# Optimization experiments

Measured on AMD Instinct MI355X. Metric: run time of the kernel, lower is better.

Reference implementation:

```python
import jax, jax.numpy as jnp
import numpy as np

NUM_HEADS = 16
KEY_SIZE = 64
HEAD_SIZE = 64


def setup_inputs() -> dict:
    key = jax.random.key(0)
    ks = jax.random.split(key, 8)
    B, S, D = 2, 2048, 1024
    s = 1.0 / np.sqrt(D)
    return {
        "q": jax.random.normal(ks[0], (B, S, D), jnp.float32),
        "k": jax.random.normal(ks[1], (B, S, D), jnp.float32),
        "v": jax.random.normal(ks[2], (B, S, D), jnp.float32),
        "v_mask": jax.random.randint(ks[3], (B, S), 0, 2, jnp.int32),
        "Wq": jax.random.normal(ks[4], (D, NUM_HEADS * KEY_SIZE), jnp.float32) * s,
        "Wk": jax.random.normal(ks[5], (D, NUM_HEADS * KEY_SIZE), jnp.float32) * s,
        "Wv": jax.random.normal(ks[6], (D, NUM_HEADS * HEAD_SIZE), jnp.float32) * s,
    }


def reference(q, k, v, v_mask, Wq, Wk, Wv):
    B, Sq, _ = q.shape
    Sk = k.shape[1]
    # projections + split heads: [B, S, H, d]
    qw = (q @ Wq).reshape(B, Sq, NUM_HEADS, KEY_SIZE)
    kw = (k @ Wk).reshape(B, Sk, NUM_HEADS, KEY_SIZE)
    vw = (v @ Wv).reshape(B, Sk, NUM_HEADS, HEAD_SIZE)
    # scores [B, H, Sq, Sk]
    a = jnp.einsum('bqhd,bkhd->bhqk', qw, kw) / np.sqrt(KEY_SIZE).astype(np.float32)
    # additive mask over key axis: x*m - (1-m)*1e12
    m = v_mask.astype(a.dtype)[:, None, None, :]
    a = a * m - (1.0 - m) * 1e12
    a = jax.nn.softmax(a, axis=-1)
    # output [B, Sq, H*head_size]
    o = jnp.einsum('bhqk,bkhd->bqhd', a, vw)
    return o.reshape(B, Sq, NUM_HEADS * HEAD_SIZE)
```

## Files before the change

### kernel.cpp

```cpp
#include <hip/hip_runtime.h>
#include <hip/hip_bf16.h>


#define SEQ 2048
#define DIM 1024
#define NPROJ 1024

typedef __bf16 bf16x8 __attribute__((ext_vector_type(8)));
typedef float floatx4 __attribute__((ext_vector_type(4)));
typedef float floatx16 __attribute__((ext_vector_type(16)));

__device__ inline unsigned short f2bf_bits(float x) {
  __hip_bfloat16 h = __float2bfloat16(x);
  return __builtin_bit_cast(unsigned short, h);
}

__device__ __forceinline__ void gload_lds16(const void* g, void* l) {
  __builtin_amdgcn_global_load_lds((const __attribute__((address_space(1))) void*)g,
                                   (__attribute__((address_space(3))) void*)l, 16, 0, 0);
}

__global__ __launch_bounds__(256) void cvt_x(
    const float* __restrict__ q, const float* __restrict__ k, const float* __restrict__ v,
    unsigned short* __restrict__ xb)
{
  const float* X = blockIdx.z == 0 ? q : (blockIdx.z == 1 ? k : v);
  unsigned short* O = xb + (size_t)blockIdx.z * 4096 * 1024;
  int i0 = blockIdx.x * 256 + threadIdx.x;
  #pragma unroll
  for (int it = 0; it < 4; ++it) {
    int i = i0 + it * 262144;
    float4 f = *reinterpret_cast<const float4*>(&X[(size_t)i * 4]);
    ushort4 o;
    o.x = f2bf_bits(f.x); o.y = f2bf_bits(f.y);
    o.z = f2bf_bits(f.z); o.w = f2bf_bits(f.w);
    *reinterpret_cast<ushort4*>(&O[(size_t)i * 4]) = o;
  }
}

__global__ __launch_bounds__(256) void transpose_w(
    const float* __restrict__ Wq, const float* __restrict__ Wk, const float* __restrict__ Wv,
    unsigned short* __restrict__ WqT, unsigned short* __restrict__ WkT, unsigned short* __restrict__ WvT)
{
  const float* W = blockIdx.z == 0 ? Wq : (blockIdx.z == 1 ? Wk : Wv);
  unsigned short* WT = blockIdx.z == 0 ? WqT : (blockIdx.z == 1 ? WkT : WvT);
  const float sc = (blockIdx.z == 0) ? 0.1803368801f : 1.0f;
  __shared__ float tile[64][65];
  const int k0 = blockIdx.x * 64;
  const int n0 = blockIdx.y * 64;
  const int t = threadIdx.x;
  #pragma unroll
  for (int it = 0; it < 4; ++it) {
    int idx = t + (it << 8);
    int r = idx >> 4, c4 = (idx & 15) << 2;
    float4 v = *reinterpret_cast<const float4*>(&W[(k0 + r) * DIM + n0 + c4]);
    tile[r][c4 + 0] = v.x; tile[r][c4 + 1] = v.y;
    tile[r][c4 + 2] = v.z; tile[r][c4 + 3] = v.w;
  }
  __syncthreads();
  #pragma unroll
  for (int it = 0; it < 4; ++it) {
    int idx = t + (it << 8);
    int r = idx >> 4, c4 = (idx & 15) << 2;
    ushort4 o;
    o.x = f2bf_bits(tile[c4 + 0][r] * sc);
    o.y = f2bf_bits(tile[c4 + 1][r] * sc);
    o.z = f2bf_bits(tile[c4 + 2][r] * sc);
    o.w = f2bf_bits(tile[c4 + 3][r] * sc);
    *reinterpret_cast<ushort4*>(&WT[(n0 + r) * DIM + k0 + c4]) = o;
  }
}

__global__ __launch_bounds__(256, 4) void proj_gemm(
    const unsigned short* __restrict__ xb,
    const unsigned short* __restrict__ WqT, const unsigned short* __restrict__ WkT,
    const unsigned short* __restrict__ WvT,
    unsigned short* __restrict__ qw, unsigned short* __restrict__ kw, unsigned short* __restrict__ vw)
{
  const unsigned short* X = xb + (size_t)blockIdx.z * 4096 * 1024;
  const unsigned short* WT = blockIdx.z == 0 ? WqT : (blockIdx.z == 1 ? WkT : WvT);
  unsigned short* Y = blockIdx.z == 0 ? qw : (blockIdx.z == 1 ? kw : vw);

  __shared__ unsigned short Al[2][128 * 32];
  __shared__ unsigned short Bl[2][128 * 32];

  const int m0 = blockIdx.x * 128, n0 = blockIdx.y * 128;
  const int t = threadIdx.x;
  const int lane = t & 63;
  const int wid = t >> 6;
  const int wm = (wid >> 1) << 6, wn = (wid & 1) << 6;
  const int qd = lane >> 4, ln = lane & 15;

  auto stage = [&](int ks, int bi) {
    const int kb = ks << 6;
    #pragma unroll
    for (int i = 0; i < 2; ++i) {
      int p = t + (i << 8);
      int r = p >> 2, c = p & 3;
      int f = (r + (r >> 2)) & 3;
      gload_lds16((const char*)X + (size_t)(m0 + r) * 2048 + kb + ((c ^ f) << 4),
                  (char*)&Al[bi][0] + p * 16);
      gload_lds16((const char*)WT + (size_t)(n0 + r) * 2048 + kb + ((c ^ f) << 4),
                  (char*)&Bl[bi][0] + p * 16);
    }
  };

  floatx4 acc[4][4] = {};
  stage(0, 0);

  for (int ks = 0; ks < 32; ++ks) {
    __syncthreads();
    if (ks + 1 < 32) stage(ks + 1, (ks + 1) & 1);
    const int bi = ks & 1;
    bf16x8 af[4], bfr[4];
    #pragma unroll
    for (int mb = 0; mb < 4; ++mb) {
      int m = wm + mb * 16 + ln;
      int fm = (m + (m >> 2)) & 3;
      af[mb] = *reinterpret_cast<const bf16x8*>(&Al[bi][m * 32 + ((qd ^ fm) << 3)]);
    }
    #pragma unroll
    for (int nb = 0; nb < 4; ++nb) {
      int n = wn + nb * 16 + ln;
      int fn = (n + (n >> 2)) & 3;
      bfr[nb] = *reinterpret_cast<const bf16x8*>(&Bl[bi][n * 32 + ((qd ^ fn) << 3)]);
    }
    #pragma unroll
    for (int mb = 0; mb < 4; ++mb)
      #pragma unroll
      for (int nb = 0; nb < 4; ++nb)
        acc[mb][nb] = __builtin_amdgcn_mfma_f32_16x16x32_bf16(af[mb], bfr[nb], acc[mb][nb], 0, 0, 0);
  }
  #pragma unroll
  for (int mb = 0; mb < 4; ++mb)
    #pragma unroll
    for (int nb = 0; nb < 4; ++nb)
      #pragma unroll
      for (int i = 0; i < 4; ++i) {
        int m = m0 + wm + mb * 16 + qd * 4 + i;
        int n = n0 + wn + nb * 16 + ln;
        Y[(size_t)m * NPROJ + n] = f2bf_bits(acc[mb][nb][i]);
      }
}

__global__ __launch_bounds__(256) void transpose_v(
    const unsigned short* __restrict__ vw, const int* __restrict__ vmask,
    unsigned short* __restrict__ vt, unsigned short* __restrict__ mb)
{
  if (blockIdx.y == 0 && blockIdx.x < 16) {
    int i = blockIdx.x * 256 + threadIdx.x;
    mb[i] = vmask[i] ? 0x3F80 : 0;
  }
  __shared__ unsigned short tile[64 * 64];
  const int t = threadIdx.x;
  const int s0 = blockIdx.x * 64;
  const int bh = blockIdx.y;
  const int b = bh >> 4, h = bh & 15;
  #pragma unroll
  for (int it = 0; it < 2; ++it) {
    int p = t + (it << 8);
    int s = p >> 3, c = p & 7;
    int cp = (c + (s >> 3) + (s & 7)) & 7;
    int4 d = *reinterpret_cast<const int4*>(&vw[(size_t)(b * SEQ + s0 + s) * NPROJ + h * 64 + c * 8]);
    if (vmask[b * SEQ + s0 + s] == 0) { d.x = 0; d.y = 0; d.z = 0; d.w = 0; }
    *reinterpret_cast<int4*>(&tile[s * 64 + cp * 8]) = d;
  }
  __syncthreads();
  #pragma unroll
  for (int it = 0; it < 2; ++it) {
    int d = (t >> 3) + (it << 5), sc = t & 7;
    struct { alignas(16) unsigned short u[8]; } o;
    #pragma unroll
    for (int j = 0; j < 8; ++j) {
      int s = sc * 8 + j;
      int cp = ((d >> 3) + (s >> 3) + (s & 7)) & 7;
      o.u[j] = tile[s * 64 + cp * 8 + (d & 7)];
    }
    *reinterpret_cast<int4*>(&vt[(size_t)(bh * 64 + d) * SEQ + s0 + sc * 8]) =
        *reinterpret_cast<const int4*>(o.u);
  }
}

__global__ __launch_bounds__(256, 3) void attn_fwd(
    const unsigned short* __restrict__ qw, const unsigned short* __restrict__ kw,
    const unsigned short* __restrict__ vt, const unsigned short* __restrict__ mb,
    float* __restrict__ out)
{
  extern __shared__ char smem[];
  unsigned short* P  = (unsigned short*)smem;
  unsigned short* Kl = (unsigned short*)(smem + 18432);
  unsigned short* Vl = (unsigned short*)(smem + 34816);
  unsigned short* Ml = (unsigned short*)(smem + 51200);

  const int t = threadIdx.x, lane = t & 63, wid = t >> 6;
  const int l5 = lane & 31, hi = lane >> 5;
  const int bh = blockIdx.x;
  const int q0 = blockIdx.y * 128;
  const int b = bh >> 4, h = bh & 15;
  const int base = b * SEQ;
  const int wq = wid * 32;

  auto stage = [&](int kt, int bi) {
    const int k0 = kt << 6;
    #pragma unroll
    for (int i = 0; i < 2; ++i) {
      int rb = wid * 16 + i * 8;
      int r = rb + (lane >> 3);
      int sw = ((lane & 7) ^ (r & 7)) << 4;
      gload_lds16((const char*)kw + ((size_t)((base + k0 + r) * NPROJ + h * 64) << 1) + sw,
                  (char*)&Kl[bi * 4096] + rb * 128);
      gload_lds16((const char*)vt + ((size_t)((bh * 64 + r) * SEQ + k0) << 1) + sw,
                  (char*)&Vl[bi * 4096] + rb * 128);
    }
    if (wid == 3 && lane < 8)
      gload_lds16((const char*)mb + ((size_t)(base + k0 + lane * 8) << 1), (char*)&Ml[bi * 64]);
  };

  #pragma unroll
  for (int i = 0; i < 4; ++i) {
    int idx = t + (i << 8);
    int r = idx >> 3, c8 = (idx & 7) << 3;
    *reinterpret_cast<int4*>(&P[r * 72 + c8]) =
        *reinterpret_cast<const int4*>(&qw[(size_t)((base + q0 + r) * NPROJ + h * 64 + c8)]);
  }
  __syncthreads();
  bf16x8 qf[4];
  #pragma unroll
  for (int kk = 0; kk < 4; ++kk)
    qf[kk] = *reinterpret_cast<const bf16x8*>(&P[(wq + l5) * 72 + kk * 16 + hi * 8]);

  floatx16 oa0 = {}, oa1 = {}, la = {};
  stage(0, 0);

  #pragma unroll 2
  for (int kt = 0; kt < SEQ / 64; ++kt) {
    __syncthreads();
    if (kt + 1 < SEQ / 64) stage(kt + 1, (kt + 1) & 1);
    const int bi = kt & 1;

    floatx16 s0 = {}, s1 = {};
    #pragma unroll
    for (int kk = 0; kk < 4; ++kk) {
      int ph = ((kk * 2 + hi) ^ (l5 & 7)) << 3;
      bf16x8 b0 = *reinterpret_cast<const bf16x8*>(&Kl[bi * 4096 + l5 * 64 + ph]);
      bf16x8 b1 = *reinterpret_cast<const bf16x8*>(&Kl[bi * 4096 + (32 + l5) * 64 + ph]);
      s0 = __builtin_amdgcn_mfma_f32_32x32x16_bf16(qf[kk], b0, s0, 0, 0, 0);
      s1 = __builtin_amdgcn_mfma_f32_32x32x16_bf16(qf[kk], b1, s1, 0, 0, 0);
    }

    #pragma unroll
    for (int r = 0; r < 16; ++r) {
      float p0 = __builtin_amdgcn_exp2f(s0[r]);
      float p1 = __builtin_amdgcn_exp2f(s1[r]);
      int row = wq + (r & 3) + ((r >> 2) << 3) + (hi << 2);
      P[row * 72 + l5] = f2bf_bits(p0);
      P[row * 72 + 32 + l5] = f2bf_bits(p1);
    }

    #pragma unroll
    for (int kk = 0; kk < 4; ++kk) {
      bf16x8 ap = *reinterpret_cast<const bf16x8*>(&P[(wq + l5) * 72 + kk * 16 + hi * 8]);
      int ph = ((kk * 2 + hi) ^ (l5 & 7)) << 3;
      bf16x8 v0 = *reinterpret_cast<const bf16x8*>(&Vl[bi * 4096 + l5 * 64 + ph]);
      bf16x8 v1 = *reinterpret_cast<const bf16x8*>(&Vl[bi * 4096 + (32 + l5) * 64 + ph]);
      bf16x8 mf = *reinterpret_cast<const bf16x8*>(&Ml[bi * 64 + kk * 16 + hi * 8]);
      oa0 = __builtin_amdgcn_mfma_f32_32x32x16_bf16(ap, v0, oa0, 0, 0, 0);
      oa1 = __builtin_amdgcn_mfma_f32_32x32x16_bf16(ap, v1, oa1, 0, 0, 0);
      la  = __builtin_amdgcn_mfma_f32_32x32x16_bf16(ap, mf, la, 0, 0, 0);
    }
  }

  #pragma unroll
  for (int r = 0; r < 16; ++r) {
    int row = wq + (r & 3) + ((r >> 2) << 3) + (hi << 2);
    float inv = 1.0f / la[r];
    size_t o = (size_t)(base + q0 + row) * NPROJ + h * 64;
    out[o + l5] = oa0[r] * inv;
    out[o + 32 + l5] = oa1[r] * inv;
  }
}

extern "C" void kernel_launch(void* const* d_in, const int* in_sizes, int n_in,
                              void* d_out, int out_size, void* d_ws, size_t ws_size,
                              hipStream_t stream) {
  const float* q  = (const float*)d_in[0];
  const float* k  = (const float*)d_in[1];
  const float* v  = (const float*)d_in[2];
  const int* vm   = (const int*)d_in[3];
  const float* Wq = (const float*)d_in[4];
  const float* Wk = (const float*)d_in[5];
  const float* Wv = (const float*)d_in[6];
  float* out = (float*)d_out;

  unsigned short* ws = (unsigned short*)d_ws;
  unsigned short* WqT = ws + ((size_t)0 << 20);
  unsigned short* WkT = ws + ((size_t)1 << 20);
  unsigned short* WvT = ws + ((size_t)2 << 20);
  unsigned short* qw  = ws + ((size_t)3 << 20);
  unsigned short* kw  = ws + ((size_t)7 << 20);
  unsigned short* vw  = ws + ((size_t)11 << 20);
  unsigned short* xb  = ws + ((size_t)15 << 20);
  unsigned short* vt  = ws + ((size_t)15 << 20);
  unsigned short* mbv = WqT;

  cvt_x<<<dim3(1024, 1, 3), 256, 0, stream>>>(q, k, v, xb);
  transpose_w<<<dim3(16, 16, 3), 256, 0, stream>>>(Wq, Wk, Wv, WqT, WkT, WvT);
  proj_gemm<<<dim3(32, 8, 3), 256, 0, stream>>>(xb, WqT, WkT, WvT, qw, kw, vw);
  transpose_v<<<dim3(32, 32), 256, 0, stream>>>(vw, vm, vt, mbv);
  attn_fwd<<<dim3(32, 16), 256, 51456, stream>>>(qw, kw, vt, mbv, out);
}
```

Baseline: 112.5 us.

## Keep softmax probabilities in registers by computing transposed scores S^T

```diff
diff --git a/kernel.cpp b/kernel.cpp
--- a/kernel.cpp
+++ b/kernel.cpp
@@ -181,16 +181,15 @@
   }
 }
 
-__global__ __launch_bounds__(256, 3) void attn_fwd(
+__global__ __launch_bounds__(256, 2) void attn_fwd(
     const unsigned short* __restrict__ qw, const unsigned short* __restrict__ kw,
     const unsigned short* __restrict__ vt, const unsigned short* __restrict__ mb,
     float* __restrict__ out)
 {
   extern __shared__ char smem[];
-  unsigned short* P  = (unsigned short*)smem;
-  unsigned short* Kl = (unsigned short*)(smem + 18432);
-  unsigned short* Vl = (unsigned short*)(smem + 34816);
-  unsigned short* Ml = (unsigned short*)(smem + 51200);
+  unsigned short* Kl = (unsigned short*)smem;
+  unsigned short* Vl = (unsigned short*)(smem + 16384);
+  unsigned short* Ml = (unsigned short*)(smem + 32768);
 
   const int t = threadIdx.x, lane = t & 63, wid = t >> 6;
   const int l5 = lane & 31, hi = lane >> 5;
@@ -206,8 +205,9 @@
     for (int i = 0; i < 2; ++i) {
       int rb = wid * 16 + i * 8;
       int r = rb + (lane >> 3);
+      int rsrc = (r & ~12) | ((r & 4) << 1) | ((r & 8) >> 1);
       int sw = ((lane & 7) ^ (r & 7)) << 4;
-      gload_lds16((const char*)kw + ((size_t)((base + k0 + r) * NPROJ + h * 64) << 1) + sw,
+      gload_lds16((const char*)kw + ((size_t)((base + k0 + rsrc) * NPROJ + h * 64) << 1) + sw,
                   (char*)&Kl[bi * 4096] + rb * 128);
       gload_lds16((const char*)vt + ((size_t)((bh * 64 + r) * SEQ + k0) << 1) + sw,
                   (char*)&Vl[bi * 4096] + rb * 128);
@@ -216,18 +216,14 @@
       gload_lds16((const char*)mb + ((size_t)(base + k0 + lane * 8) << 1), (char*)&Ml[bi * 64]);
   };
 
-  #pragma unroll
-  for (int i = 0; i < 4; ++i) {
-    int idx = t + (i << 8);
-    int r = idx >> 3, c8 = (idx & 7) << 3;
-    *reinterpret_cast<int4*>(&P[r * 72 + c8]) =
-        *reinterpret_cast<const int4*>(&qw[(size_t)((base + q0 + r) * NPROJ + h * 64 + c8)]);
-  }
-  __syncthreads();
   bf16x8 qf[4];
-  #pragma unroll
-  for (int kk = 0; kk < 4; ++kk)
-    qf[kk] = *reinterpret_cast<const bf16x8*>(&P[(wq + l5) * 72 + kk * 16 + hi * 8]);
+  {
+    const unsigned short* qptr =
+        qw + (size_t)(base + q0 + wq + l5) * NPROJ + h * 64 + hi * 8;
+    #pragma unroll
+    for (int kk = 0; kk < 4; ++kk)
+      qf[kk] = *reinterpret_cast<const bf16x8*>(qptr + kk * 16);
+  }
 
   floatx16 oa0 = {}, oa1 = {}, la = {};
   stage(0, 0);
@@ -242,31 +238,32 @@
     #pragma unroll
     for (int kk = 0; kk < 4; ++kk) {
       int ph = ((kk * 2 + hi) ^ (l5 & 7)) << 3;
-      bf16x8 b0 = *reinterpret_cast<const bf16x8*>(&Kl[bi * 4096 + l5 * 64 + ph]);
-      bf16x8 b1 = *reinterpret_cast<const bf16x8*>(&Kl[bi * 4096 + (32 + l5) * 64 + ph]);
-      s0 = __builtin_amdgcn_mfma_f32_32x32x16_bf16(qf[kk], b0, s0, 0, 0, 0);
-      s1 = __builtin_amdgcn_mfma_f32_32x32x16_bf16(qf[kk], b1, s1, 0, 0, 0);
-    }
-
+      bf16x8 k0f = *reinterpret_cast<const bf16x8*>(&Kl[bi * 4096 + l5 * 64 + ph]);
+      bf16x8 k1f = *reinterpret_cast<const bf16x8*>(&Kl[bi * 4096 + (32 + l5) * 64 + ph]);
+      s0 = __builtin_amdgcn_mfma_f32_32x32x16_bf16(k0f, qf[kk], s0, 0, 0, 0);
+      s1 = __builtin_amdgcn_mfma_f32_32x32x16_bf16(k1f, qf[kk], s1, 0, 0, 0);
+    }
+
+    float pe[32];
     #pragma unroll
     for (int r = 0; r < 16; ++r) {
-      float p0 = __builtin_amdgcn_exp2f(s0[r]);
-      float p1 = __builtin_amdgcn_exp2f(s1[r]);
-      int row = wq + (r & 3) + ((r >> 2) << 3) + (hi << 2);
-      P[row * 72 + l5] = f2bf_bits(p0);
-      P[row * 72 + 32 + l5] = f2bf_bits(p1);
+      pe[r]      = __builtin_amdgcn_exp2f(s0[r]);
+      pe[16 + r] = __builtin_amdgcn_exp2f(s1[r]);
     }
 
     #pragma unroll
     for (int kk = 0; kk < 4; ++kk) {
-      bf16x8 ap = *reinterpret_cast<const bf16x8*>(&P[(wq + l5) * 72 + kk * 16 + hi * 8]);
+      struct alignas(16) { unsigned short u[8]; } pk;
+      #pragma unroll
+      for (int j = 0; j < 8; ++j) pk.u[j] = f2bf_bits(pe[8 * kk + j]);
+      bf16x8 pa = __builtin_bit_cast(bf16x8, pk);
       int ph = ((kk * 2 + hi) ^ (l5 & 7)) << 3;
       bf16x8 v0 = *reinterpret_cast<const bf16x8*>(&Vl[bi * 4096 + l5 * 64 + ph]);
       bf16x8 v1 = *reinterpret_cast<const bf16x8*>(&Vl[bi * 4096 + (32 + l5) * 64 + ph]);
       bf16x8 mf = *reinterpret_cast<const bf16x8*>(&Ml[bi * 64 + kk * 16 + hi * 8]);
-      oa0 = __builtin_amdgcn_mfma_f32_32x32x16_bf16(ap, v0, oa0, 0, 0, 0);
-      oa1 = __builtin_amdgcn_mfma_f32_32x32x16_bf16(ap, v1, oa1, 0, 0, 0);
-      la  = __builtin_amdgcn_mfma_f32_32x32x16_bf16(ap, mf, la, 0, 0, 0);
+      oa0 = __builtin_amdgcn_mfma_f32_32x32x16_bf16(pa, v0, oa0, 0, 0, 0);
+      oa1 = __builtin_amdgcn_mfma_f32_32x32x16_bf16(pa, v1, oa1, 0, 0, 0);
+      la  = __builtin_amdgcn_mfma_f32_32x32x16_bf16(pa, mf, la, 0, 0, 0);
     }
   }
 
@@ -307,5 +304,5 @@
   transpose_w<<<dim3(16, 16, 3), 256, 0, stream>>>(Wq, Wk, Wv, WqT, WkT, WvT);
   proj_gemm<<<dim3(32, 8, 3), 256, 0, stream>>>(xb, WqT, WkT, WvT, qw, kw, vw);
   transpose_v<<<dim3(32, 32), 256, 0, stream>>>(vw, vm, vt, mbv);
-  attn_fwd<<<dim3(32, 16), 256, 51456, stream>>>(qw, kw, vt, mbv, out);
-}
+  attn_fwd<<<dim3(32, 16), 256, 33024, stream>>>(qw, kw, vt, mbv, out);
+}
```

New measurement: 101.4 us. 1.11x faster.
